# Optimization experiments

Hardware: AMD Instinct MI355X
Metric: run time of the kernel (lower is better)

Reference implementation:

```python
import math
import jax, jax.numpy as jnp
import numpy as np

D, NH, NL, NP = 256, 8, 3, 4
HD = D // NH
SHAPES = np.array([[92, 92], [46, 46], [23, 23]], dtype=np.int32)
LSI = np.concatenate([[0], np.cumsum(SHAPES[:, 0] * SHAPES[:, 1])[:-1]]).astype(np.int32)
LV = int((SHAPES[:, 0] * SHAPES[:, 1]).sum())  # 11109
B, LQ = 2, LV


def setup_inputs() -> dict:
    key = jax.random.key(0)
    ks = jax.random.split(key, 8)
    query = jax.random.normal(ks[0], (B, LQ, D), jnp.float32)
    reference_points = jax.random.uniform(ks[1], (B, LQ, NL, 2), dtype=jnp.float32)
    value_flat = jax.random.normal(ks[2], (B, LV, D), jnp.float32)
    # sampling_offsets: small random weight + structured directional bias (as in _reset_parameters)
    W_off = jax.random.normal(ks[3], (D, NH * NL * NP * 2), jnp.float32) * 0.01
    thetas = np.arange(NH, dtype=np.float64) * (2.0 * math.pi / NH)
    g = np.stack([np.cos(thetas), np.sin(thetas)], axis=-1)
    g = g / np.abs(g).max(axis=-1, keepdims=True)
    g = np.tile(g[:, None, None, :], (1, NL, NP, 1))
    g = g * (np.arange(NP) + 1)[None, None, :, None]
    b_off = jnp.asarray(g.reshape(-1), jnp.float32)
    W_attn = jax.random.normal(ks[4], (D, NH * NL * NP), jnp.float32) * 0.01
    b_attn = jnp.zeros((NH * NL * NP,), jnp.float32)
    W_val = jax.random.normal(ks[5], (D, D), jnp.float32) * (1.0 / math.sqrt(D))
    b_val = jnp.zeros((D,), jnp.float32)
    W_out = jax.random.normal(ks[6], (D, D), jnp.float32) * (1.0 / math.sqrt(D))
    b_out = jnp.zeros((D,), jnp.float32)
    return dict(query=query, reference_points=reference_points, value_flat=value_flat,
                W_val=W_val, b_val=b_val, W_off=W_off, b_off=b_off,
                W_attn=W_attn, b_attn=b_attn, W_out=W_out, b_out=b_out,
                spatial_shapes=jnp.asarray(SHAPES), level_start_index=jnp.asarray(LSI))


def _bilinear_sample(val_l, grid):
    """torch.F.grid_sample(mode='bilinear', padding_mode='zeros', align_corners=False).
    val_l: [B,H,W,nH,hd]; grid: [B,Q,nH,P,2] with (x,y) in [-1,1].
    Returns [B,nH,Q,P,hd]."""
    Bq, H, W, nH, hd = val_l.shape
    Q, P = grid.shape[1], grid.shape[3]
    x = ((grid[..., 0] + 1.0) * W - 1.0) * 0.5   # pixel coords, align_corners=False
    y = ((grid[..., 1] + 1.0) * H - 1.0) * 0.5
    x0f, y0f = jnp.floor(x), jnp.floor(y)
    lx, ly = x - x0f, y - y0f
    x0, y0 = x0f.astype(jnp.int32), y0f.astype(jnp.int32)
    val_bh = val_l.transpose(0, 3, 1, 2, 4).reshape(Bq * nH, H * W, hd)

    def corner(yi, xi, w):
        valid = (xi >= 0) & (xi < W) & (yi >= 0) & (yi < H)
        idx = jnp.clip(yi, 0, H - 1) * W + jnp.clip(xi, 0, W - 1)   # [B,Q,nH,P]
        idx_bh = idx.transpose(0, 2, 1, 3).reshape(Bq * nH, Q * P)
        g = jnp.take_along_axis(val_bh, idx_bh[:, :, None], axis=1)  # [B*nH, Q*P, hd]
        wm = (w * valid.astype(w.dtype)).transpose(0, 2, 1, 3).reshape(Bq * nH, Q * P, 1)
        return g * wm

    out = (corner(y0, x0, (1 - ly) * (1 - lx)) + corner(y0, x0 + 1, (1 - ly) * lx)
           + corner(y0 + 1, x0, ly * (1 - lx)) + corner(y0 + 1, x0 + 1, ly * lx))
    return out.reshape(Bq, nH, Q, P, hd)


def reference(query, reference_points, value_flat, W_val, b_val, W_off, b_off,
              W_attn, b_attn, W_out, b_out, spatial_shapes, level_start_index):
    shapes = np.asarray(spatial_shapes)          # static level geometry
    starts = np.asarray(level_start_index)
    Bq, Lq, _ = query.shape
    value = (value_flat @ W_val + b_val).reshape(Bq, -1, NH, HD)
    off = (query @ W_off + b_off).reshape(Bq, Lq, NH, NL, NP, 2)        # (dy,dx) pixels
    aw = jax.nn.softmax((query @ W_attn + b_attn).reshape(Bq, Lq, NH, NL * NP), axis=-1)
    aw = aw.reshape(Bq, Lq, NH, NL, NP)
    sh_f = jnp.asarray(shapes, jnp.float32)                              # [L,2] = (H,W)
    norm_off = off / sh_f[None, None, None, :, None, :]
    loc = reference_points[:, :, None, :, None, :] + norm_off           # [B,Lq,NH,NL,NP,2] (y,x)
    grid = 2.0 * loc[..., ::-1] - 1.0                                    # (x,y) in [-1,1]
    out = jnp.zeros((Bq, Lq, NH, HD), query.dtype)
    for l in range(NL):
        H, W = int(shapes[l, 0]), int(shapes[l, 1])
        s = int(starts[l])
        val_l = value[:, s:s + H * W].reshape(Bq, H, W, NH, HD)
        sampled = _bilinear_sample(val_l, grid[:, :, :, l])              # [B,NH,Lq,NP,HD]
        out = out + jnp.einsum('bhqpc,bqhp->bqhc', sampled, aw[:, :, :, l])
    return out.reshape(Bq, Lq, D) @ W_out + b_out
```

## Files before the change

kernel.cpp:

```cpp
#include <hip/hip_runtime.h>

#define LQn   11109
#define Bn    2
#define MTOT  (Bn * LQn)

typedef __attribute__((ext_vector_type(8))) short short8;
typedef __attribute__((ext_vector_type(4))) float f32x4;

__device__ __forceinline__ unsigned short f2bf(float f) {
  union { float f; unsigned int u; } v; v.f = f;
  unsigned int r = v.u + 0x7fffu + ((v.u >> 16) & 1u);
  return (unsigned short)(r >> 16);
}
__device__ __forceinline__ float bf2f(unsigned short u) {
  union { unsigned int u; float f; } v; v.u = ((unsigned int)u) << 16;
  return v.f;
}

__global__ __launch_bounds__(256) void cast4_kernel(const float* __restrict__ src,
                                                    unsigned short* __restrict__ dst,
                                                    int n4) {
  int i = blockIdx.x * 256 + threadIdx.x;
  if (i >= n4) return;
  float4 v = ((const float4*)src)[i];
  ushort4 o;
  o.x = f2bf(v.x); o.y = f2bf(v.y); o.z = f2bf(v.z); o.w = f2bf(v.w);
  ((ushort4*)dst)[i] = o;
}

__global__ __launch_bounds__(256) void prep_weights(
    const float* __restrict__ Wval, const float* __restrict__ Woff,
    const float* __restrict__ Wattn, const float* __restrict__ Wout,
    const float* __restrict__ boff, const float* __restrict__ battn,
    unsigned short* __restrict__ Wval_t, unsigned short* __restrict__ Wcat_t,
    unsigned short* __restrict__ Wout_t, float* __restrict__ bcat) {
  int i = blockIdx.x * 256 + threadIdx.x;
  int n = i >> 8, k = i & 255;
  if (n < 256) {
    Wval_t[i] = f2bf(Wval[k * 256 + n]);
    Wout_t[i] = f2bf(Wout[k * 256 + n]);
  }
  float src = (n < 192) ? Woff[k * 192 + n] : Wattn[k * 96 + (n - 192)];
  Wcat_t[i] = f2bf(src);
  if (i < 288) bcat[i] = (i < 192) ? boff[i] : battn[i - 192];
}

template <bool BF16OUT>
__global__ __launch_bounds__(256) void gemm_bf16_64x64(
    const unsigned short* __restrict__ A,
    const unsigned short* __restrict__ Bt,
    const float* __restrict__ bias,
    void* __restrict__ Cout,
    int M, int N) {
  __shared__ unsigned short As[64][40];
  __shared__ unsigned short Bs[64][40];

  const int t = threadIdx.x;
  const int bm = blockIdx.x, bn = blockIdx.y;
  const int wave = t >> 6, lane = t & 63;
  const int wm = wave >> 1, wn = wave & 1;
  const int quad = lane >> 4, l16 = lane & 15;

  const int ldr = t >> 2;
  const int ldk = (t & 3) * 8;
  const int arow = bm * 64 + ldr;
  const int brow = bn * 64 + ldr;

  f32x4 acc[2][2];
  for (int i = 0; i < 2; i++)
    for (int j = 0; j < 2; j++) acc[i][j] = (f32x4){0.f, 0.f, 0.f, 0.f};

  for (int kb = 0; kb < 8; kb++) {
    const int k0 = kb * 32;
    uint4 av = {0u, 0u, 0u, 0u}, bv = {0u, 0u, 0u, 0u};
    if (arow < M) av = *(const uint4*)(A + (size_t)arow * 256 + k0 + ldk);
    if (brow < N) bv = *(const uint4*)(Bt + (size_t)brow * 256 + k0 + ldk);
    __syncthreads();
    *(uint4*)(&As[ldr][ldk]) = av;
    *(uint4*)(&Bs[ldr][ldk]) = bv;
    __syncthreads();
    short8 af[2], bfr[2];
    for (int i = 0; i < 2; i++)
      af[i] = *(const short8*)(&As[wm * 32 + i * 16 + l16][quad * 8]);
    for (int j = 0; j < 2; j++)
      bfr[j] = *(const short8*)(&Bs[wn * 32 + j * 16 + l16][quad * 8]);
    for (int i = 0; i < 2; i++)
      for (int j = 0; j < 2; j++)
        acc[i][j] = __builtin_amdgcn_mfma_f32_16x16x32_bf16(af[i], bfr[j], acc[i][j], 0, 0, 0);
  }

  for (int i = 0; i < 2; i++)
    for (int j = 0; j < 2; j++) {
      int colg = bn * 64 + wn * 32 + j * 16 + l16;
      if (colg >= N) continue;
      float bsv = bias[colg];
      int row0 = bm * 64 + wm * 32 + i * 16 + quad * 4;
      for (int r = 0; r < 4; r++) {
        int rg = row0 + r;
        if (rg < M) {
          float v = acc[i][j][r] + bsv;
          if (BF16OUT) ((unsigned short*)Cout)[(size_t)rg * N + colg] = f2bf(v);
          else         ((float*)Cout)[(size_t)rg * N + colg] = v;
        }
      }
    }
}

__global__ __launch_bounds__(256) void msda_sample2(
    const unsigned short* __restrict__ value,
    const float* __restrict__ logits,
    const float* __restrict__ refp,
    unsigned short* __restrict__ sampled) {
  __shared__ float lg[4][288];
  __shared__ float rfs[4][6];
  __shared__ float tw[4][96][4];
  __shared__ int   ti[4][96][4];

  const int t = threadIdx.x;
  const int ql = t >> 6;
  const int lane = t & 63;
  const int bq = blockIdx.x * 4 + ql;
  const bool qvalid = bq < MTOT;

  if (qvalid) {
    for (int i = lane; i < 288; i += 64) lg[ql][i] = logits[(size_t)bq * 288 + i];
    if (lane < 6) rfs[ql][lane] = refp[(size_t)bq * 6 + lane];
  }
  __syncthreads();

  if (qvalid) {
    const int Hs[3] = {92, 46, 23};
    const int Ss[3] = {0, 8464, 10580};
    for (int s = lane; s < 96; s += 64) {
      const int h = s / 12;
      const int pl = s - h * 12;
      const int l = pl >> 2;
      const int H = Hs[l], W = Hs[l], S = Ss[l];
      float mx = -1e30f;
#pragma unroll
      for (int i = 0; i < 12; i++) mx = fmaxf(mx, lg[ql][192 + h * 12 + i]);
      float den = 0.f;
#pragma unroll
      for (int i = 0; i < 12; i++) den += __expf(lg[ql][192 + h * 12 + i] - mx);
      const float aw = __expf(lg[ql][192 + s] - mx) / den;

      const float offy = lg[ql][2 * s], offx = lg[ql][2 * s + 1];
      const float x = rfs[ql][l * 2 + 1] * W + offx - 0.5f;
      const float y = rfs[ql][l * 2 + 0] * H + offy - 0.5f;
      const float xf = floorf(x), yf = floorf(y);
      const int x0 = (int)xf, y0 = (int)yf;
      const float lx = x - xf, ly = y - yf;
      const bool xv0 = (x0 >= 0) & (x0 < W), xv1 = (x0 + 1 >= 0) & (x0 + 1 < W);
      const bool yv0 = (y0 >= 0) & (y0 < H), yv1 = (y0 + 1 >= 0) & (y0 + 1 < H);
      const int xc0 = min(max(x0, 0), W - 1), xc1 = min(max(x0 + 1, 0), W - 1);
      const int yc0 = min(max(y0, 0), H - 1), yc1 = min(max(y0 + 1, 0), H - 1);
      ti[ql][s][0] = S + yc0 * W + xc0;
      ti[ql][s][1] = S + yc0 * W + xc1;
      ti[ql][s][2] = S + yc1 * W + xc0;
      ti[ql][s][3] = S + yc1 * W + xc1;
      tw[ql][s][0] = (yv0 & xv0) ? aw * (1.f - ly) * (1.f - lx) : 0.f;
      tw[ql][s][1] = (yv0 & xv1) ? aw * (1.f - ly) * lx : 0.f;
      tw[ql][s][2] = (yv1 & xv0) ? aw * ly * (1.f - lx) : 0.f;
      tw[ql][s][3] = (yv1 & xv1) ? aw * ly * lx : 0.f;
    }
  }
  __syncthreads();

  if (qvalid) {
    const int h = lane >> 3, cg = lane & 7;
    const int coff = h * 32 + cg * 4;
    const unsigned short* vb = value + (size_t)(bq / LQn) * LQn * 256 + coff;
    float a0 = 0.f, a1 = 0.f, a2 = 0.f, a3 = 0.f;
#pragma unroll
    for (int p = 0; p < 12; p++) {
      const int s = h * 12 + p;
      const f32x4 wv = *(const f32x4*)(&tw[ql][s][0]);
      const int4 iv = *(const int4*)(&ti[ql][s][0]);
#pragma unroll
      for (int k = 0; k < 4; k++) {
        const int idx = (k == 0) ? iv.x : (k == 1) ? iv.y : (k == 2) ? iv.z : iv.w;
        const float w = wv[k];
        const ushort4 u = *(const ushort4*)(vb + (size_t)idx * 256);
        a0 += w * bf2f(u.x);
        a1 += w * bf2f(u.y);
        a2 += w * bf2f(u.z);
        a3 += w * bf2f(u.w);
      }
    }
    ushort4 o;
    o.x = f2bf(a0); o.y = f2bf(a1); o.z = f2bf(a2); o.w = f2bf(a3);
    *(ushort4*)(sampled + (size_t)bq * 256 + coff) = o;
  }
}

extern "C" void kernel_launch(void* const* d_in, const int* in_sizes, int n_in,
                              void* d_out, int out_size, void* d_ws, size_t ws_size,
                              hipStream_t stream) {
  const float* query      = (const float*)d_in[0];
  const float* refp       = (const float*)d_in[1];
  const float* value_flat = (const float*)d_in[2];
  const float* W_val      = (const float*)d_in[3];
  const float* b_val      = (const float*)d_in[4];
  const float* W_off      = (const float*)d_in[5];
  const float* b_off      = (const float*)d_in[6];
  const float* W_attn     = (const float*)d_in[7];
  const float* b_attn     = (const float*)d_in[8];
  const float* W_out      = (const float*)d_in[9];
  const float* b_out      = (const float*)d_in[10];

  char* w = (char*)d_ws;
  size_t o = 0;
  auto carve = [&](size_t bytes) -> void* {
    void* p = (void*)(w + o);
    o += (bytes + 255) & ~(size_t)255;
    return p;
  };
  unsigned short* q_bf    = (unsigned short*)carve((size_t)MTOT * 256 * 2);
  unsigned short* v_bf    = (unsigned short*)carve((size_t)MTOT * 256 * 2);
  unsigned short* Wval_t  = (unsigned short*)carve(256 * 256 * 2);
  unsigned short* Wcat_t  = (unsigned short*)carve(288 * 256 * 2);
  unsigned short* Wout_t  = (unsigned short*)carve(256 * 256 * 2);
  float*          bcat    = (float*)carve(288 * 4);
  unsigned short* value16 = (unsigned short*)carve((size_t)MTOT * 256 * 2);
  float*          logits  = (float*)carve((size_t)MTOT * 288 * 4);
  unsigned short* samp_bf = (unsigned short*)carve((size_t)MTOT * 256 * 2);

  const int n4 = MTOT * 256 / 4;
  const int cgrid = (n4 + 255) / 256;
  cast4_kernel<<<cgrid, 256, 0, stream>>>(query, q_bf, n4);
  cast4_kernel<<<cgrid, 256, 0, stream>>>(value_flat, v_bf, n4);
  prep_weights<<<288, 256, 0, stream>>>(W_val, W_off, W_attn, W_out, b_off, b_attn,
                                        Wval_t, Wcat_t, Wout_t, bcat);

  const int mg = (MTOT + 63) / 64;
  dim3 g1(mg, 4);
  gemm_bf16_64x64<true><<<g1, 256, 0, stream>>>(v_bf, Wval_t, b_val, value16, MTOT, 256);
  dim3 g2(mg, 5);
  gemm_bf16_64x64<false><<<g2, 256, 0, stream>>>(q_bf, Wcat_t, bcat, logits, MTOT, 288);

  const int sgrid = (MTOT + 3) / 4;
  msda_sample2<<<sgrid, 256, 0, stream>>>(value16, logits, refp, samp_bf);

  dim3 g3(mg, 4);
  gemm_bf16_64x64<false><<<g3, 256, 0, stream>>>(samp_bf, Wout_t, b_out, (float*)d_out, MTOT, 256);
}
```

Before: 201.6 us.

## Fuse fp32-to-bf16 casts into GEMMs, merge projection GEMMs, use head-major value layout

Removes the separate cast kernels: the fused GEMM loads fp32 query and value directly and converts them to bf16 while staging into shared memory. The value and offset/attention projections run as one launch with a 9-column-block grid. The value projection writes a head-major [B][head][pos][32] layout so each head's gathered rows are contiguous, and the sampler precomputes per-head softmax max and reciprocal once and uses shifted byte offsets. This saves two full passes over the inputs and one launch, at the cost of reading fp32 A tiles (twice the bytes per tile) inside the GEMM and scattered 2-byte stores in the value epilogue.

```diff
diff --git a/kernel.cpp b/kernel.cpp
--- a/kernel.cpp
+++ b/kernel.cpp
@@ -11,21 +11,6 @@
   union { float f; unsigned int u; } v; v.f = f;
   unsigned int r = v.u + 0x7fffu + ((v.u >> 16) & 1u);
   return (unsigned short)(r >> 16);
-}
-__device__ __forceinline__ float bf2f(unsigned short u) {
-  union { unsigned int u; float f; } v; v.u = ((unsigned int)u) << 16;
-  return v.f;
-}
-
-__global__ __launch_bounds__(256) void cast4_kernel(const float* __restrict__ src,
-                                                    unsigned short* __restrict__ dst,
-                                                    int n4) {
-  int i = blockIdx.x * 256 + threadIdx.x;
-  if (i >= n4) return;
-  float4 v = ((const float4*)src)[i];
-  ushort4 o;
-  o.x = f2bf(v.x); o.y = f2bf(v.y); o.z = f2bf(v.z); o.w = f2bf(v.w);
-  ((ushort4*)dst)[i] = o;
 }
 
 __global__ __launch_bounds__(256) void prep_weights(
@@ -45,13 +30,93 @@
   if (i < 288) bcat[i] = (i < 192) ? boff[i] : battn[i - 192];
 }
 
-template <bool BF16OUT>
-__global__ __launch_bounds__(256) void gemm_bf16_64x64(
+__global__ __launch_bounds__(256) void gemm_fused12(
+    const float* __restrict__ Aval,
+    const float* __restrict__ Aq,
+    const unsigned short* __restrict__ Bval,
+    const unsigned short* __restrict__ Bcat,
+    const float* __restrict__ bval, const float* __restrict__ bcat,
+    unsigned short* __restrict__ value16,
+    float* __restrict__ logits) {
+  __shared__ unsigned short As[64][40];
+  __shared__ unsigned short Bs[64][40];
+
+  const int bm = blockIdx.x;
+  int bn = blockIdx.y;
+  const bool is2 = bn >= 4;
+  if (is2) bn -= 4;
+  const float* __restrict__ A = is2 ? Aq : Aval;
+  const unsigned short* __restrict__ Bt = is2 ? Bcat : Bval;
+  const float* __restrict__ bias = is2 ? bcat : bval;
+  const int N = is2 ? 288 : 256;
+
+  const int t = threadIdx.x;
+  const int wave = t >> 6, lane = t & 63;
+  const int wm = wave >> 1, wn = wave & 1;
+  const int quad = lane >> 4, l16 = lane & 15;
+
+  const int ldr = t >> 2;
+  const int ldk = (t & 3) * 8;
+  const int arow = bm * 64 + ldr;
+  const int brow = bn * 64 + ldr;
+
+  f32x4 acc[2][2];
+  for (int i = 0; i < 2; i++)
+    for (int j = 0; j < 2; j++) acc[i][j] = (f32x4){0.f, 0.f, 0.f, 0.f};
+
+  for (int kb = 0; kb < 8; kb++) {
+    const int k0 = kb * 32;
+    float4 a0 = {0.f, 0.f, 0.f, 0.f}, a1 = a0;
+    uint4 bv = {0u, 0u, 0u, 0u};
+    if (arow < MTOT) {
+      a0 = *(const float4*)(A + (size_t)arow * 256 + k0 + ldk);
+      a1 = *(const float4*)(A + (size_t)arow * 256 + k0 + ldk + 4);
+    }
+    if (brow < N) bv = *(const uint4*)(Bt + (size_t)brow * 256 + k0 + ldk);
+    ushort4 lo, hi;
+    lo.x = f2bf(a0.x); lo.y = f2bf(a0.y); lo.z = f2bf(a0.z); lo.w = f2bf(a0.w);
+    hi.x = f2bf(a1.x); hi.y = f2bf(a1.y); hi.z = f2bf(a1.z); hi.w = f2bf(a1.w);
+    __syncthreads();
+    *(ushort4*)(&As[ldr][ldk]) = lo;
+    *(ushort4*)(&As[ldr][ldk + 4]) = hi;
+    *(uint4*)(&Bs[ldr][ldk]) = bv;
+    __syncthreads();
+    short8 af[2], bfr[2];
+    for (int i = 0; i < 2; i++)
+      af[i] = *(const short8*)(&As[wm * 32 + i * 16 + l16][quad * 8]);
+    for (int j = 0; j < 2; j++)
+      bfr[j] = *(const short8*)(&Bs[wn * 32 + j * 16 + l16][quad * 8]);
+    for (int i = 0; i < 2; i++)
+      for (int j = 0; j < 2; j++)
+        acc[i][j] = __builtin_amdgcn_mfma_f32_16x16x32_bf16(af[i], bfr[j], acc[i][j], 0, 0, 0);
+  }
+
+  for (int i = 0; i < 2; i++)
+    for (int j = 0; j < 2; j++) {
+      int colg = bn * 64 + wn * 32 + j * 16 + l16;
+      if (colg >= N) continue;
+      float bsv = bias[colg];
+      int row0 = bm * 64 + wm * 32 + i * 16 + quad * 4;
+      for (int r = 0; r < 4; r++) {
+        int rg = row0 + r;
+        if (rg >= MTOT) continue;
+        float v = acc[i][j][r] + bsv;
+        if (is2) {
+          logits[(size_t)rg * 288 + colg] = v;
+        } else {
+          int b = (rg >= LQn) ? 1 : 0;
+          int p = rg - b * LQn;
+          value16[((size_t)(b * 8 + (colg >> 5)) * LQn + p) * 32 + (colg & 31)] = f2bf(v);
+        }
+      }
+    }
+}
+
+__global__ __launch_bounds__(256) void gemm_a16(
     const unsigned short* __restrict__ A,
     const unsigned short* __restrict__ Bt,
     const float* __restrict__ bias,
-    void* __restrict__ Cout,
-    int M, int N) {
+    float* __restrict__ C) {
   __shared__ unsigned short As[64][40];
   __shared__ unsigned short Bs[64][40];
 
@@ -73,8 +138,8 @@
   for (int kb = 0; kb < 8; kb++) {
     const int k0 = kb * 32;
     uint4 av = {0u, 0u, 0u, 0u}, bv = {0u, 0u, 0u, 0u};
-    if (arow < M) av = *(const uint4*)(A + (size_t)arow * 256 + k0 + ldk);
-    if (brow < N) bv = *(const uint4*)(Bt + (size_t)brow * 256 + k0 + ldk);
+    if (arow < MTOT) av = *(const uint4*)(A + (size_t)arow * 256 + k0 + ldk);
+    bv = *(const uint4*)(Bt + (size_t)brow * 256 + k0 + ldk);
     __syncthreads();
     *(uint4*)(&As[ldr][ldk]) = av;
     *(uint4*)(&Bs[ldr][ldk]) = bv;
@@ -92,104 +157,110 @@
   for (int i = 0; i < 2; i++)
     for (int j = 0; j < 2; j++) {
       int colg = bn * 64 + wn * 32 + j * 16 + l16;
-      if (colg >= N) continue;
       float bsv = bias[colg];
       int row0 = bm * 64 + wm * 32 + i * 16 + quad * 4;
       for (int r = 0; r < 4; r++) {
         int rg = row0 + r;
-        if (rg < M) {
-          float v = acc[i][j][r] + bsv;
-          if (BF16OUT) ((unsigned short*)Cout)[(size_t)rg * N + colg] = f2bf(v);
-          else         ((float*)Cout)[(size_t)rg * N + colg] = v;
-        }
+        if (rg < MTOT) C[(size_t)rg * 256 + colg] = acc[i][j][r] + bsv;
       }
     }
 }
 
-__global__ __launch_bounds__(256) void msda_sample2(
-    const unsigned short* __restrict__ value,
+__global__ __launch_bounds__(256) void msda_sample3(
+    const unsigned short* __restrict__ value16,
     const float* __restrict__ logits,
     const float* __restrict__ refp,
     unsigned short* __restrict__ sampled) {
   __shared__ float lg[4][288];
   __shared__ float rfs[4][6];
+  __shared__ float hmx[4][8], hrd[4][8];
   __shared__ float tw[4][96][4];
-  __shared__ int   ti[4][96][4];
+  __shared__ unsigned int ti[4][96][4];
 
   const int t = threadIdx.x;
   const int ql = t >> 6;
   const int lane = t & 63;
   const int bq = blockIdx.x * 4 + ql;
-  const bool qvalid = bq < MTOT;
-
-  if (qvalid) {
+  const bool qv = bq < MTOT;
+
+  if (qv) {
     for (int i = lane; i < 288; i += 64) lg[ql][i] = logits[(size_t)bq * 288 + i];
     if (lane < 6) rfs[ql][lane] = refp[(size_t)bq * 6 + lane];
   }
   __syncthreads();
 
-  if (qvalid) {
+  if (qv && lane < 8) {
+    float mx = -1e30f;
+#pragma unroll
+    for (int i = 0; i < 12; i++) mx = fmaxf(mx, lg[ql][192 + lane * 12 + i]);
+    float den = 0.f;
+#pragma unroll
+    for (int i = 0; i < 12; i++) den += __expf(lg[ql][192 + lane * 12 + i] - mx);
+    hmx[ql][lane] = mx;
+    hrd[ql][lane] = 1.0f / den;
+  }
+  __syncthreads();
+
+  if (qv) {
     const int Hs[3] = {92, 46, 23};
     const int Ss[3] = {0, 8464, 10580};
-    for (int s = lane; s < 96; s += 64) {
-      const int h = s / 12;
-      const int pl = s - h * 12;
-      const int l = pl >> 2;
-      const int H = Hs[l], W = Hs[l], S = Ss[l];
-      float mx = -1e30f;
-#pragma unroll
-      for (int i = 0; i < 12; i++) mx = fmaxf(mx, lg[ql][192 + h * 12 + i]);
-      float den = 0.f;
-#pragma unroll
-      for (int i = 0; i < 12; i++) den += __expf(lg[ql][192 + h * 12 + i] - mx);
-      const float aw = __expf(lg[ql][192 + s] - mx) / den;
-
-      const float offy = lg[ql][2 * s], offx = lg[ql][2 * s + 1];
-      const float x = rfs[ql][l * 2 + 1] * W + offx - 0.5f;
-      const float y = rfs[ql][l * 2 + 0] * H + offy - 0.5f;
-      const float xf = floorf(x), yf = floorf(y);
-      const int x0 = (int)xf, y0 = (int)yf;
-      const float lx = x - xf, ly = y - yf;
-      const bool xv0 = (x0 >= 0) & (x0 < W), xv1 = (x0 + 1 >= 0) & (x0 + 1 < W);
-      const bool yv0 = (y0 >= 0) & (y0 < H), yv1 = (y0 + 1 >= 0) & (y0 + 1 < H);
-      const int xc0 = min(max(x0, 0), W - 1), xc1 = min(max(x0 + 1, 0), W - 1);
-      const int yc0 = min(max(y0, 0), H - 1), yc1 = min(max(y0 + 1, 0), H - 1);
-      ti[ql][s][0] = S + yc0 * W + xc0;
-      ti[ql][s][1] = S + yc0 * W + xc1;
-      ti[ql][s][2] = S + yc1 * W + xc0;
-      ti[ql][s][3] = S + yc1 * W + xc1;
-      tw[ql][s][0] = (yv0 & xv0) ? aw * (1.f - ly) * (1.f - lx) : 0.f;
-      tw[ql][s][1] = (yv0 & xv1) ? aw * (1.f - ly) * lx : 0.f;
-      tw[ql][s][2] = (yv1 & xv0) ? aw * ly * (1.f - lx) : 0.f;
-      tw[ql][s][3] = (yv1 & xv1) ? aw * ly * lx : 0.f;
+#pragma unroll
+    for (int rnd = 0; rnd < 2; rnd++) {
+      const int s = lane + rnd * 64;
+      if (s < 96) {
+        const int h = s / 12;
+        const int pl = s - h * 12;
+        const int l = pl >> 2;
+        const int H = Hs[l], W = Hs[l], S = Ss[l];
+        const float aw = __expf(lg[ql][192 + s] - hmx[ql][h]) * hrd[ql][h];
+        const float offy = lg[ql][2 * s], offx = lg[ql][2 * s + 1];
+        const float x = rfs[ql][l * 2 + 1] * W + offx - 0.5f;
+        const float y = rfs[ql][l * 2 + 0] * H + offy - 0.5f;
+        const float xf = floorf(x), yf = floorf(y);
+        const int x0 = (int)xf, y0 = (int)yf;
+        const float lx = x - xf, ly = y - yf;
+        const bool xv0 = (x0 >= 0) & (x0 < W), xv1 = (x0 + 1 >= 0) & (x0 + 1 < W);
+        const bool yv0 = (y0 >= 0) & (y0 < H), yv1 = (y0 + 1 >= 0) & (y0 + 1 < H);
+        const int xc0 = min(max(x0, 0), W - 1), xc1 = min(max(x0 + 1, 0), W - 1);
+        const int yc0 = min(max(y0, 0), H - 1), yc1 = min(max(y0 + 1, 0), H - 1);
+        ti[ql][s][0] = (unsigned)(S + yc0 * W + xc0) << 6;
+        ti[ql][s][1] = (unsigned)(S + yc0 * W + xc1) << 6;
+        ti[ql][s][2] = (unsigned)(S + yc1 * W + xc0) << 6;
+        ti[ql][s][3] = (unsigned)(S + yc1 * W + xc1) << 6;
+        tw[ql][s][0] = (yv0 & xv0) ? aw * (1.f - ly) * (1.f - lx) : 0.f;
+        tw[ql][s][1] = (yv0 & xv1) ? aw * (1.f - ly) * lx : 0.f;
+        tw[ql][s][2] = (yv1 & xv0) ? aw * ly * (1.f - lx) : 0.f;
+        tw[ql][s][3] = (yv1 & xv1) ? aw * ly * lx : 0.f;
+      }
     }
   }
   __syncthreads();
 
-  if (qvalid) {
+  if (qv) {
     const int h = lane >> 3, cg = lane & 7;
-    const int coff = h * 32 + cg * 4;
-    const unsigned short* vb = value + (size_t)(bq / LQn) * LQn * 256 + coff;
+    const unsigned laneoff = (unsigned)h * (LQn * 64u) + (unsigned)cg * 8u;
+    const char* __restrict__ vb =
+        (const char*)(value16 + (size_t)(bq / LQn) * (8u * LQn * 32u));
     float a0 = 0.f, a1 = 0.f, a2 = 0.f, a3 = 0.f;
 #pragma unroll
     for (int p = 0; p < 12; p++) {
       const int s = h * 12 + p;
       const f32x4 wv = *(const f32x4*)(&tw[ql][s][0]);
-      const int4 iv = *(const int4*)(&ti[ql][s][0]);
+      const uint4 iv = *(const uint4*)(&ti[ql][s][0]);
 #pragma unroll
       for (int k = 0; k < 4; k++) {
-        const int idx = (k == 0) ? iv.x : (k == 1) ? iv.y : (k == 2) ? iv.z : iv.w;
+        const unsigned tib = (k == 0) ? iv.x : (k == 1) ? iv.y : (k == 2) ? iv.z : iv.w;
         const float w = wv[k];
-        const ushort4 u = *(const ushort4*)(vb + (size_t)idx * 256);
-        a0 += w * bf2f(u.x);
-        a1 += w * bf2f(u.y);
-        a2 += w * bf2f(u.z);
-        a3 += w * bf2f(u.w);
+        const uint2 u = *(const uint2*)(vb + (laneoff + tib));
+        a0 += w * __uint_as_float(u.x << 16);
+        a1 += w * __uint_as_float(u.x & 0xffff0000u);
+        a2 += w * __uint_as_float(u.y << 16);
+        a3 += w * __uint_as_float(u.y & 0xffff0000u);
       }
     }
     ushort4 o;
     o.x = f2bf(a0); o.y = f2bf(a1); o.z = f2bf(a2); o.w = f2bf(a3);
-    *(ushort4*)(sampled + (size_t)bq * 256 + coff) = o;
+    *(ushort4*)(sampled + (size_t)bq * 256 + h * 32 + cg * 4) = o;
   }
 }
 
@@ -215,8 +286,6 @@
     o += (bytes + 255) & ~(size_t)255;
     return p;
   };
-  unsigned short* q_bf    = (unsigned short*)carve((size_t)MTOT * 256 * 2);
-  unsigned short* v_bf    = (unsigned short*)carve((size_t)MTOT * 256 * 2);
   unsigned short* Wval_t  = (unsigned short*)carve(256 * 256 * 2);
   unsigned short* Wcat_t  = (unsigned short*)carve(288 * 256 * 2);
   unsigned short* Wout_t  = (unsigned short*)carve(256 * 256 * 2);
@@ -225,22 +294,17 @@
   float*          logits  = (float*)carve((size_t)MTOT * 288 * 4);
   unsigned short* samp_bf = (unsigned short*)carve((size_t)MTOT * 256 * 2);
 
-  const int n4 = MTOT * 256 / 4;
-  const int cgrid = (n4 + 255) / 256;
-  cast4_kernel<<<cgrid, 256, 0, stream>>>(query, q_bf, n4);
-  cast4_kernel<<<cgrid, 256, 0, stream>>>(value_flat, v_bf, n4);
   prep_weights<<<288, 256, 0, stream>>>(W_val, W_off, W_attn, W_out, b_off, b_attn,
                                         Wval_t, Wcat_t, Wout_t, bcat);
 
   const int mg = (MTOT + 63) / 64;
-  dim3 g1(mg, 4);
-  gemm_bf16_64x64<true><<<g1, 256, 0, stream>>>(v_bf, Wval_t, b_val, value16, MTOT, 256);
-  dim3 g2(mg, 5);
-  gemm_bf16_64x64<false><<<g2, 256, 0, stream>>>(q_bf, Wcat_t, bcat, logits, MTOT, 288);
+  dim3 g12(mg, 9);
+  gemm_fused12<<<g12, 256, 0, stream>>>(value_flat, query, Wval_t, Wcat_t,
+                                        b_val, bcat, value16, logits);
 
   const int sgrid = (MTOT + 3) / 4;
-  msda_sample2<<<sgrid, 256, 0, stream>>>(value16, logits, refp, samp_bf);
+  msda_sample3<<<sgrid, 256, 0, stream>>>(value16, logits, refp, samp_bf);
 
   dim3 g3(mg, 4);
-  gemm_bf16_64x64<false><<<g3, 256, 0, stream>>>(samp_bf, Wout_t, b_out, (float*)d_out, MTOT, 256);
-}
+  gemm_a16<<<g3, 256, 0, stream>>>(samp_bf, Wout_t, b_out, (float*)d_out);
+}
```

Result: faster. 195.0 us (-3.3%).
